# Performance work log

Hardware: AMD Instinct MI355X
Metric: run time of the kernel (lower is better)

The kernel has to match this reference:

```python
import jax, jax.numpy as jnp
import numpy as np

NROW = 200000
R = 32
B = 131072
NDIM = 3
STEP = 0.01  # stepsize from optimize() default step=lambda x: 0.01


def setup_inputs() -> dict:
    key = jax.random.key(0)
    ks = jax.random.split(key, 12)
    inp = {}
    for d in range(NDIM):
        # positive entries (like torch.rand) keep phi > 0
        inp[f"U{d}"] = jax.random.uniform(ks[d], (NROW, R), dtype=jnp.float32, minval=0.05, maxval=1.0)
        inp[f"S{d}"] = jax.random.uniform(ks[3 + d], (NROW, R), dtype=jnp.float32)
        inp[f"T{d}"] = jax.random.uniform(ks[6 + d], (NROW, R), dtype=jnp.float32)
    inp["L"] = jax.random.uniform(ks[9], (R,), dtype=jnp.float32, minval=0.1, maxval=1.0)
    inp["batch_vals"] = jax.random.randint(ks[10], (B,), 0, 2).astype(jnp.float32)  # binary data
    inp["batch_entries"] = jax.random.randint(ks[11], (B, NDIM), 0, NROW)
    return inp


def _em_update(U, S, T, L, batch_vals, batch_entries):
    # U, S, T: (ndim, nrow, R); batch_entries: (B, ndim); batch_vals: (B,)
    idx = batch_entries.T  # (ndim, B)
    g = jax.vmap(lambda u, i: u[i])(U, idx)  # gathered rows: (ndim, B, R)
    # c_vectors[dim] = L * prod of OTHER dims' gathered vectors
    prod_others = jnp.stack([g[1] * g[2], g[0] * g[2], g[0] * g[1]])  # (ndim, B, R)
    c = L * prod_others  # (ndim, B, R)
    p = g[0] * g[1] * g[2]  # (B, R) full elementwise product
    phi = jnp.sum(L * p, axis=-1)  # (B,)
    # d_vectors[dim, b, r] = phi[b] - L[r] * p[b, r]  (same for every dim)
    d_vec = (phi[:, None] - L * p)[None]  # (1, B, R)
    # expectation step (binary): E[wi] = 0.5/phi * tanh(phi/2)
    wi = 0.5 / phi * jnp.tanh(phi / 2.0)  # (B,)
    ki = batch_vals - 0.5  # (B,)
    wi_b = wi[None, :, None]
    s_upd = c * c * wi_b  # (ndim, B, R)
    t_upd = (ki[None, :, None] - d_vec * wi_b) * c  # (ndim, B, R)
    seg = lambda dat, i: jax.ops.segment_sum(dat, i, num_segments=NROW)
    s_acc = jax.vmap(seg)(s_upd, idx)  # (ndim, NROW, R)
    t_acc = jax.vmap(seg)(t_upd, idx)
    cnt = jax.vmap(seg)(jnp.ones(idx.shape, jnp.float32), idx)  # (ndim, NROW)
    touched = (cnt > 0)[..., None]
    # EMA write-back only to rows that appeared in the batch
    S_new = jnp.where(touched, (1.0 - STEP) * S + STEP * s_acc, S)
    T_new = jnp.where(touched, (1.0 - STEP) * T + STEP * t_acc, T)
    return jnp.stack([S_new, T_new])  # (2, ndim, NROW, R)


def reference(U0, U1, U2, S0, S1, S2, T0, T1, T2, L, batch_vals, batch_entries):
    U = jnp.stack([U0, U1, U2])
    S = jnp.stack([S0, S1, S2])
    T = jnp.stack([T0, T1, T2])
    return _em_update(U, S, T, L, batch_vals, batch_entries)
```

## Files before the change

### kernel.cpp

```cpp
#include <hip/hip_runtime.h>

#define NROW 200000
#define RDIM 32
#define BATCH 131072
#define STEP 0.01f


__global__ __launch_bounds__(256) void em_pre(
    const float* __restrict__ U0, const float* __restrict__ U1,
    const float* __restrict__ U2, const float* __restrict__ L,
    const float* __restrict__ bv, const int* __restrict__ be,
    int* __restrict__ head, int* __restrict__ nxt,
    float2* __restrict__ scal, float* __restrict__ LpBuf)
{
    int tid = blockIdx.x * blockDim.x + threadIdx.x;
    int i   = tid >> 3;
    int sub = tid & 7;
    if (i >= BATCH) return;

    int e0 = be[i * 3 + 0];
    int e1 = be[i * 3 + 1];
    int e2 = be[i * 3 + 2];

    float4 g0 = *(const float4*)(U0 + (size_t)e0 * RDIM + sub * 4);
    float4 g1 = *(const float4*)(U1 + (size_t)e1 * RDIM + sub * 4);
    float4 g2 = *(const float4*)(U2 + (size_t)e2 * RDIM + sub * 4);
    float4 Lv = *(const float4*)(L + sub * 4);

    float4 Lp;
    Lp.x = Lv.x * g0.x * g1.x * g2.x;
    Lp.y = Lv.y * g0.y * g1.y * g2.y;
    Lp.z = Lv.z * g0.z * g1.z * g2.z;
    Lp.w = Lv.w * g0.w * g1.w * g2.w;

    float phi = (Lp.x + Lp.y) + (Lp.z + Lp.w);
    phi += __shfl_xor(phi, 1);
    phi += __shfl_xor(phi, 2);
    phi += __shfl_xor(phi, 4);

    float wi = 0.5f / phi * tanhf(0.5f * phi);

    *(float4*)(LpBuf + (size_t)i * RDIM + sub * 4) = Lp;

    if (sub == 0) {
        float A = (bv[i] - 0.5f) - phi * wi;
        scal[i] = make_float2(A, wi);
    }
    if (sub < 3) {
        int row = (sub == 0) ? e0 : (sub == 1) ? e1 : e2;
        int idx = i * 3 + sub;
        nxt[idx] = atomicExch(&head[sub * NROW + row], idx);
    }
}

__global__ __launch_bounds__(256) void em_apply_vec(
    const float* __restrict__ U0, const float* __restrict__ U1,
    const float* __restrict__ U2,
    const float* __restrict__ S0, const float* __restrict__ S1,
    const float* __restrict__ S2,
    const float* __restrict__ T0, const float* __restrict__ T1,
    const float* __restrict__ T2,
    const int* __restrict__ head, const int* __restrict__ nxt,
    const float2* __restrict__ scal, const float* __restrict__ LpBuf,
    float* __restrict__ out)
{
    int tid = blockIdx.x * blockDim.x + threadIdx.x;
    int rid = tid >> 3;
    int sub = tid & 7;
    if (rid >= 3 * NROW) return;

    int d   = rid / NROW;
    int row = rid - d * NROW;

    const float* Ud   = (d == 0) ? U0 : (d == 1) ? U1 : U2;
    const float* Ssrc = (d == 0) ? S0 : (d == 1) ? S1 : S2;
    const float* Tsrc = (d == 0) ? T0 : (d == 1) ? T1 : T2;

    size_t roff = (size_t)row * RDIM + sub * 4;
    float4 s_in = *(const float4*)(Ssrc + roff);
    float4 t_in = *(const float4*)(Tsrc + roff);

    int    t    = head[rid];
    float4 oS   = s_in;
    float4 oT   = t_in;

    if (t != -1) {
        float4 gd = *(const float4*)(Ud + roff);
        float4 rg;
        rg.x = __builtin_amdgcn_rcpf(gd.x);
        rg.y = __builtin_amdgcn_rcpf(gd.y);
        rg.z = __builtin_amdgcn_rcpf(gd.z);
        rg.w = __builtin_amdgcn_rcpf(gd.w);

        float4 sa = make_float4(0.f, 0.f, 0.f, 0.f);
        float4 ta = make_float4(0.f, 0.f, 0.f, 0.f);
        while (t != -1) {
            int e = t / 3;
            float2 aw = scal[e];
            float4 Lp = *(const float4*)(LpBuf + (size_t)e * RDIM + sub * 4);
            float cx = Lp.x * rg.x, cy = Lp.y * rg.y,
                  cz = Lp.z * rg.z, cw = Lp.w * rg.w;
            sa.x += aw.y * cx * cx;  sa.y += aw.y * cy * cy;
            sa.z += aw.y * cz * cz;  sa.w += aw.y * cw * cw;
            ta.x += (aw.x + aw.y * Lp.x) * cx;
            ta.y += (aw.x + aw.y * Lp.y) * cy;
            ta.z += (aw.x + aw.y * Lp.z) * cz;
            ta.w += (aw.x + aw.y * Lp.w) * cw;
            t = nxt[t];
        }
        oS.x = (1.0f - STEP) * s_in.x + STEP * sa.x;
        oS.y = (1.0f - STEP) * s_in.y + STEP * sa.y;
        oS.z = (1.0f - STEP) * s_in.z + STEP * sa.z;
        oS.w = (1.0f - STEP) * s_in.w + STEP * sa.w;
        oT.x = (1.0f - STEP) * t_in.x + STEP * ta.x;
        oT.y = (1.0f - STEP) * t_in.y + STEP * ta.y;
        oT.z = (1.0f - STEP) * t_in.z + STEP * ta.z;
        oT.w = (1.0f - STEP) * t_in.w + STEP * ta.w;
    }

    size_t offS = ((size_t)d * NROW + row) * RDIM + sub * 4;
    *(float4*)(out + offS) = oS;
    *(float4*)(out + (size_t)3 * NROW * RDIM + offS) = oT;
}

__global__ __launch_bounds__(256) void em_build(
    const int* __restrict__ be, int* __restrict__ head, int* __restrict__ nxt)
{
    int tid = blockIdx.x * blockDim.x + threadIdx.x;
    if (tid >= BATCH * 3) return;
    int d   = tid % 3;
    int row = be[tid];
    nxt[tid] = atomicExch(&head[d * NROW + row], tid);
}

__global__ __launch_bounds__(256) void em_gather(
    const float* __restrict__ U0, const float* __restrict__ U1,
    const float* __restrict__ U2,
    const float* __restrict__ S0, const float* __restrict__ S1,
    const float* __restrict__ S2,
    const float* __restrict__ T0, const float* __restrict__ T1,
    const float* __restrict__ T2,
    const float* __restrict__ L,  const float* __restrict__ bv,
    const int* __restrict__ be,
    const int* __restrict__ head, const int* __restrict__ nxt,
    float* __restrict__ out)
{
    int gid   = blockIdx.x * blockDim.x + threadIdx.x;
    int group = gid >> 5;
    int lane  = gid & 31;
    if (group >= 3 * NROW) return;

    int d   = group / NROW;
    int row = group - d * NROW;

    const float* Ud  = (d == 0) ? U0 : (d == 1) ? U1 : U2;
    const float* Uo1 = (d == 0) ? U1 : U0;
    const float* Uo2 = (d == 2) ? U1 : U2;
    int o1 = (d == 0) ? 1 : 0;
    int o2 = (d == 2) ? 1 : 2;
    const float* Ssrc = (d == 0) ? S0 : (d == 1) ? S1 : S2;
    const float* Tsrc = (d == 0) ? T0 : (d == 1) ? T1 : T2;

    size_t row_off = (size_t)row * RDIM + lane;
    float s_in = Ssrc[row_off];
    float t_in = Tsrc[row_off];

    int   t    = head[group];
    float outS = s_in;
    float outT = t_in;

    if (t != -1) {
        float Lr = L[lane];
        float gd = Ud[row_off];
        float sacc = 0.0f, tacc = 0.0f;
        while (t != -1) {
            int e  = t / 3;
            int r1 = be[e * 3 + o1];
            int r2 = be[e * 3 + o2];
            float g1 = Uo1[(size_t)r1 * RDIM + lane];
            float g2 = Uo2[(size_t)r2 * RDIM + lane];
            float ki = bv[e] - 0.5f;

            float c   = Lr * g1 * g2;
            float Lp  = c * gd;
            float phi = Lp;
            #pragma unroll
            for (int m = 1; m < 32; m <<= 1) phi += __shfl_xor(phi, m);

            float wi = 0.5f / phi * tanhf(0.5f * phi);
            sacc += c * c * wi;
            tacc += (ki - (phi - Lp) * wi) * c;

            t = nxt[t];
        }
        outS = (1.0f - STEP) * s_in + STEP * sacc;
        outT = (1.0f - STEP) * t_in + STEP * tacc;
    }

    size_t offS = ((size_t)d * NROW + row) * RDIM + lane;
    out[offS] = outS;
    out[(size_t)3 * NROW * RDIM + offS] = outT;
}

extern "C" void kernel_launch(void* const* d_in, const int* in_sizes, int n_in,
                              void* d_out, int out_size, void* d_ws, size_t ws_size,
                              hipStream_t stream)
{
    const float* U0 = (const float*)d_in[0];
    const float* S0 = (const float*)d_in[1];
    const float* T0 = (const float*)d_in[2];
    const float* U1 = (const float*)d_in[3];
    const float* S1 = (const float*)d_in[4];
    const float* T1 = (const float*)d_in[5];
    const float* U2 = (const float*)d_in[6];
    const float* S2 = (const float*)d_in[7];
    const float* T2 = (const float*)d_in[8];
    const float* L  = (const float*)d_in[9];
    const float* bv = (const float*)d_in[10];
    const int*   be = (const int*)d_in[11];

    float* out = (float*)d_out;

    const size_t head_n = (size_t)3 * NROW;
    const size_t nxt_n  = (size_t)3 * BATCH;
    const size_t ws_fast = (head_n + nxt_n) * sizeof(int)
                         + (size_t)BATCH * sizeof(float2)
                         + (size_t)BATCH * RDIM * sizeof(float);

    int* head_ = (int*)d_ws;
    int* nxt   = head_ + head_n;

    hipMemsetAsync(head_, 0xFF, head_n * sizeof(int), stream);

    if (ws_size >= ws_fast) {
        float2* scal  = (float2*)(nxt + nxt_n);
        float*  LpBuf = (float*)(scal + BATCH);

        int pblocks = (BATCH * 8 + 255) / 256;
        em_pre<<<pblocks, 256, 0, stream>>>(U0, U1, U2, L, bv, be,
                                            head_, nxt, scal, LpBuf);

        long athreads = 3L * NROW * 8;
        int  ablocks  = (int)((athreads + 255) / 256);
        em_apply_vec<<<ablocks, 256, 0, stream>>>(U0, U1, U2, S0, S1, S2,
                                                  T0, T1, T2, head_, nxt,
                                                  scal, LpBuf, out);
    } else {
        int bblocks = (BATCH * 3 + 255) / 256;
        em_build<<<bblocks, 256, 0, stream>>>(be, head_, nxt);

        long gthreads = 3L * NROW * 32;
        int  gblocks  = (int)((gthreads + 255) / 256);
        em_gather<<<gblocks, 256, 0, stream>>>(U0, U1, U2, S0, S1, S2,
                                               T0, T1, T2, L, bv, be,
                                               head_, nxt, out);
    }
}
```

Baseline: 107.8 us.

## Replace per-row linked lists with fixed-capacity buckets plus overflow chain

Builds per-row fixed-capacity buckets (up to 8 batch indices) via atomicAdd counters during the precompute pass, falling back to the existing linked list only for overflow entries. The apply kernel iterates the bucket contiguously instead of chasing nxt pointers, meant to remove dependent-load latency. It adds an extra memset for counters and a larger workspace footprint, and drops the low-workspace gather fallback path.

Measured after the change: 118.9 us. 10.3% more time.

```diff
diff --git a/kernel.cpp b/kernel.cpp
--- a/kernel.cpp
+++ b/kernel.cpp
@@ -4,7 +4,151 @@
 #define RDIM 32
 #define BATCH 131072
 #define STEP 0.01f
-
+#define CAP 8
+
+
+__global__ __launch_bounds__(256) void em_pre_bkt(
+    const float* __restrict__ U0, const float* __restrict__ U1,
+    const float* __restrict__ U2, const float* __restrict__ L,
+    const float* __restrict__ bv, const int* __restrict__ be,
+    int* __restrict__ cnt, int* __restrict__ head, int* __restrict__ nxt,
+    int* __restrict__ bucket, float2* __restrict__ scal, float* __restrict__ LpBuf)
+{
+    int tid = blockIdx.x * blockDim.x + threadIdx.x;
+    int i   = tid >> 3;
+    int sub = tid & 7;
+    if (i >= BATCH) return;
+
+    int e0 = be[i * 3 + 0];
+    int e1 = be[i * 3 + 1];
+    int e2 = be[i * 3 + 2];
+
+    float4 g0 = *(const float4*)(U0 + (size_t)e0 * RDIM + sub * 4);
+    float4 g1 = *(const float4*)(U1 + (size_t)e1 * RDIM + sub * 4);
+    float4 g2 = *(const float4*)(U2 + (size_t)e2 * RDIM + sub * 4);
+    float4 Lv = *(const float4*)(L + sub * 4);
+
+    float4 Lp;
+    Lp.x = Lv.x * g0.x * g1.x * g2.x;
+    Lp.y = Lv.y * g0.y * g1.y * g2.y;
+    Lp.z = Lv.z * g0.z * g1.z * g2.z;
+    Lp.w = Lv.w * g0.w * g1.w * g2.w;
+
+    float phi = (Lp.x + Lp.y) + (Lp.z + Lp.w);
+    phi += __shfl_xor(phi, 1);
+    phi += __shfl_xor(phi, 2);
+    phi += __shfl_xor(phi, 4);
+
+    float wi = 0.5f / phi * tanhf(0.5f * phi);
+
+    *(float4*)(LpBuf + (size_t)i * RDIM + sub * 4) = Lp;
+
+    if (sub == 0) {
+        float A = (bv[i] - 0.5f) - phi * wi;
+        scal[i] = make_float2(A, wi);
+    }
+    if (sub < 3) {
+        int row = (sub == 0) ? e0 : (sub == 1) ? e1 : e2;
+        int rid = sub * NROW + row;
+        int slot = atomicAdd(&cnt[rid], 1);
+        if (slot < CAP) {
+            bucket[(size_t)rid * CAP + slot] = i;
+        } else {
+            int idx = i * 3 + sub;
+            nxt[idx] = atomicExch(&head[rid], idx);
+        }
+    }
+}
+
+__global__ __launch_bounds__(256) void em_apply_bkt(
+    const float* __restrict__ U0, const float* __restrict__ U1,
+    const float* __restrict__ U2,
+    const float* __restrict__ S0, const float* __restrict__ S1,
+    const float* __restrict__ S2,
+    const float* __restrict__ T0, const float* __restrict__ T1,
+    const float* __restrict__ T2,
+    const int* __restrict__ cnt, const int* __restrict__ head,
+    const int* __restrict__ nxt, const int* __restrict__ bucket,
+    const float2* __restrict__ scal, const float* __restrict__ LpBuf,
+    float* __restrict__ out)
+{
+    int tid = blockIdx.x * blockDim.x + threadIdx.x;
+    int rid = tid >> 3;
+    int sub = tid & 7;
+    if (rid >= 3 * NROW) return;
+
+    int d   = rid / NROW;
+    int row = rid - d * NROW;
+
+    const float* Ud   = (d == 0) ? U0 : (d == 1) ? U1 : U2;
+    const float* Ssrc = (d == 0) ? S0 : (d == 1) ? S1 : S2;
+    const float* Tsrc = (d == 0) ? T0 : (d == 1) ? T1 : T2;
+
+    size_t roff = (size_t)row * RDIM + sub * 4;
+    float4 s_in = *(const float4*)(Ssrc + roff);
+    float4 t_in = *(const float4*)(Tsrc + roff);
+
+    int    n  = cnt[rid];
+    float4 oS = s_in;
+    float4 oT = t_in;
+
+    if (n > 0) {
+        float4 gd = *(const float4*)(Ud + roff);
+        float4 rg;
+        rg.x = __builtin_amdgcn_rcpf(gd.x);
+        rg.y = __builtin_amdgcn_rcpf(gd.y);
+        rg.z = __builtin_amdgcn_rcpf(gd.z);
+        rg.w = __builtin_amdgcn_rcpf(gd.w);
+
+        float4 sa = make_float4(0.f, 0.f, 0.f, 0.f);
+        float4 ta = make_float4(0.f, 0.f, 0.f, 0.f);
+
+        const int* bk = bucket + (size_t)rid * CAP;
+        int nb = (n < CAP) ? n : CAP;
+        for (int j = 0; j < nb; ++j) {
+            int e = bk[j];
+            float2 aw = scal[e];
+            float4 Lp = *(const float4*)(LpBuf + (size_t)e * RDIM + sub * 4);
+            float cx = Lp.x * rg.x, cy = Lp.y * rg.y,
+                  cz = Lp.z * rg.z, cw = Lp.w * rg.w;
+            sa.x += aw.y * cx * cx;  sa.y += aw.y * cy * cy;
+            sa.z += aw.y * cz * cz;  sa.w += aw.y * cw * cw;
+            ta.x += (aw.x + aw.y * Lp.x) * cx;
+            ta.y += (aw.x + aw.y * Lp.y) * cy;
+            ta.z += (aw.x + aw.y * Lp.z) * cz;
+            ta.w += (aw.x + aw.y * Lp.w) * cw;
+        }
+        if (n > CAP) {
+            int t = head[rid];
+            while (t != -1) {
+                int e = t / 3;
+                float2 aw = scal[e];
+                float4 Lp = *(const float4*)(LpBuf + (size_t)e * RDIM + sub * 4);
+                float cx = Lp.x * rg.x, cy = Lp.y * rg.y,
+                      cz = Lp.z * rg.z, cw = Lp.w * rg.w;
+                sa.x += aw.y * cx * cx;  sa.y += aw.y * cy * cy;
+                sa.z += aw.y * cz * cz;  sa.w += aw.y * cw * cw;
+                ta.x += (aw.x + aw.y * Lp.x) * cx;
+                ta.y += (aw.x + aw.y * Lp.y) * cy;
+                ta.z += (aw.x + aw.y * Lp.z) * cz;
+                ta.w += (aw.x + aw.y * Lp.w) * cw;
+                t = nxt[t];
+            }
+        }
+        oS.x = (1.0f - STEP) * s_in.x + STEP * sa.x;
+        oS.y = (1.0f - STEP) * s_in.y + STEP * sa.y;
+        oS.z = (1.0f - STEP) * s_in.z + STEP * sa.z;
+        oS.w = (1.0f - STEP) * s_in.w + STEP * sa.w;
+        oT.x = (1.0f - STEP) * t_in.x + STEP * ta.x;
+        oT.y = (1.0f - STEP) * t_in.y + STEP * ta.y;
+        oT.z = (1.0f - STEP) * t_in.z + STEP * ta.z;
+        oT.w = (1.0f - STEP) * t_in.w + STEP * ta.w;
+    }
+
+    size_t offS = ((size_t)d * NROW + row) * RDIM + sub * 4;
+    *(float4*)(out + offS) = oS;
+    *(float4*)(out + (size_t)3 * NROW * RDIM + offS) = oT;
+}
 
 __global__ __launch_bounds__(256) void em_pre(
     const float* __restrict__ U0, const float* __restrict__ U1,
@@ -80,9 +224,9 @@
     float4 s_in = *(const float4*)(Ssrc + roff);
     float4 t_in = *(const float4*)(Tsrc + roff);
 
-    int    t    = head[rid];
-    float4 oS   = s_in;
-    float4 oT   = t_in;
+    int    t  = head[rid];
+    float4 oS = s_in;
+    float4 oT = t_in;
 
     if (t != -1) {
         float4 gd = *(const float4*)(Ud + roff);
@@ -123,85 +267,6 @@
     *(float4*)(out + (size_t)3 * NROW * RDIM + offS) = oT;
 }
 
-__global__ __launch_bounds__(256) void em_build(
-    const int* __restrict__ be, int* __restrict__ head, int* __restrict__ nxt)
-{
-    int tid = blockIdx.x * blockDim.x + threadIdx.x;
-    if (tid >= BATCH * 3) return;
-    int d   = tid % 3;
-    int row = be[tid];
-    nxt[tid] = atomicExch(&head[d * NROW + row], tid);
-}
-
-__global__ __launch_bounds__(256) void em_gather(
-    const float* __restrict__ U0, const float* __restrict__ U1,
-    const float* __restrict__ U2,
-    const float* __restrict__ S0, const float* __restrict__ S1,
-    const float* __restrict__ S2,
-    const float* __restrict__ T0, const float* __restrict__ T1,
-    const float* __restrict__ T2,
-    const float* __restrict__ L,  const float* __restrict__ bv,
-    const int* __restrict__ be,
-    const int* __restrict__ head, const int* __restrict__ nxt,
-    float* __restrict__ out)
-{
-    int gid   = blockIdx.x * blockDim.x + threadIdx.x;
-    int group = gid >> 5;
-    int lane  = gid & 31;
-    if (group >= 3 * NROW) return;
-
-    int d   = group / NROW;
-    int row = group - d * NROW;
-
-    const float* Ud  = (d == 0) ? U0 : (d == 1) ? U1 : U2;
-    const float* Uo1 = (d == 0) ? U1 : U0;
-    const float* Uo2 = (d == 2) ? U1 : U2;
-    int o1 = (d == 0) ? 1 : 0;
-    int o2 = (d == 2) ? 1 : 2;
-    const float* Ssrc = (d == 0) ? S0 : (d == 1) ? S1 : S2;
-    const float* Tsrc = (d == 0) ? T0 : (d == 1) ? T1 : T2;
-
-    size_t row_off = (size_t)row * RDIM + lane;
-    float s_in = Ssrc[row_off];
-    float t_in = Tsrc[row_off];
-
-    int   t    = head[group];
-    float outS = s_in;
-    float outT = t_in;
-
-    if (t != -1) {
-        float Lr = L[lane];
-        float gd = Ud[row_off];
-        float sacc = 0.0f, tacc = 0.0f;
-        while (t != -1) {
-            int e  = t / 3;
-            int r1 = be[e * 3 + o1];
-            int r2 = be[e * 3 + o2];
-            float g1 = Uo1[(size_t)r1 * RDIM + lane];
-            float g2 = Uo2[(size_t)r2 * RDIM + lane];
-            float ki = bv[e] - 0.5f;
-
-            float c   = Lr * g1 * g2;
-            float Lp  = c * gd;
-            float phi = Lp;
-            #pragma unroll
-            for (int m = 1; m < 32; m <<= 1) phi += __shfl_xor(phi, m);
-
-            float wi = 0.5f / phi * tanhf(0.5f * phi);
-            sacc += c * c * wi;
-            tacc += (ki - (phi - Lp) * wi) * c;
-
-            t = nxt[t];
-        }
-        outS = (1.0f - STEP) * s_in + STEP * sacc;
-        outT = (1.0f - STEP) * t_in + STEP * tacc;
-    }
-
-    size_t offS = ((size_t)d * NROW + row) * RDIM + lane;
-    out[offS] = outS;
-    out[(size_t)3 * NROW * RDIM + offS] = outT;
-}
-
 extern "C" void kernel_launch(void* const* d_in, const int* in_sizes, int n_in,
                               void* d_out, int out_size, void* d_ws, size_t ws_size,
                               hipStream_t stream)
@@ -221,20 +286,46 @@
 
     float* out = (float*)d_out;
 
-    const size_t head_n = (size_t)3 * NROW;
+    const size_t rows3  = (size_t)3 * NROW;
     const size_t nxt_n  = (size_t)3 * BATCH;
-    const size_t ws_fast = (head_n + nxt_n) * sizeof(int)
-                         + (size_t)BATCH * sizeof(float2)
-                         + (size_t)BATCH * RDIM * sizeof(float);
-
-    int* head_ = (int*)d_ws;
-    int* nxt   = head_ + head_n;
-
-    hipMemsetAsync(head_, 0xFF, head_n * sizeof(int), stream);
+    const size_t bkt_n  = rows3 * CAP;
+
+    const size_t ints_fast = rows3  + rows3  + nxt_n + bkt_n;
+    const size_t ws_fast   = ints_fast * sizeof(int)
+                           + (size_t)BATCH * sizeof(float2)
+                           + (size_t)BATCH * RDIM * sizeof(float);
+    const size_t ws_mid    = (rows3 + nxt_n) * sizeof(int)
+                           + (size_t)BATCH * sizeof(float2)
+                           + (size_t)BATCH * RDIM * sizeof(float);
 
     if (ws_size >= ws_fast) {
+        int*    cnt    = (int*)d_ws;
+        int*    head_  = cnt + rows3;
+        int*    nxt    = head_ + rows3;
+        int*    bucket = nxt + nxt_n;
+        float2* scal   = (float2*)(bucket + bkt_n);
+        float*  LpBuf  = (float*)(scal + BATCH);
+
+        hipMemsetAsync(cnt, 0, rows3 * sizeof(int), stream);
+        hipMemsetAsync(head_, 0xFF, rows3 * sizeof(int), stream);
+
+        int pblocks = (BATCH * 8 + 255) / 256;
+        em_pre_bkt<<<pblocks, 256, 0, stream>>>(U0, U1, U2, L, bv, be,
+                                                cnt, head_, nxt, bucket,
+                                                scal, LpBuf);
+
+        long athreads = 3L * NROW * 8;
+        int  ablocks  = (int)((athreads + 255) / 256);
+        em_apply_bkt<<<ablocks, 256, 0, stream>>>(U0, U1, U2, S0, S1, S2,
+                                                  T0, T1, T2, cnt, head_, nxt,
+                                                  bucket, scal, LpBuf, out);
+    } else if (ws_size >= ws_mid) {
+        int*    head_ = (int*)d_ws;
+        int*    nxt   = head_ + rows3;
         float2* scal  = (float2*)(nxt + nxt_n);
         float*  LpBuf = (float*)(scal + BATCH);
+
+        hipMemsetAsync(head_, 0xFF, rows3 * sizeof(int), stream);
 
         int pblocks = (BATCH * 8 + 255) / 256;
         em_pre<<<pblocks, 256, 0, stream>>>(U0, U1, U2, L, bv, be,
@@ -245,14 +336,5 @@
         em_apply_vec<<<ablocks, 256, 0, stream>>>(U0, U1, U2, S0, S1, S2,
                                                   T0, T1, T2, head_, nxt,
                                                   scal, LpBuf, out);
-    } else {
-        int bblocks = (BATCH * 3 + 255) / 256;
-        em_build<<<bblocks, 256, 0, stream>>>(be, head_, nxt);
-
-        long gthreads = 3L * NROW * 32;
-        int  gblocks  = (int)((gthreads + 255) / 256);
-        em_gather<<<gblocks, 256, 0, stream>>>(U0, U1, U2, S0, S1, S2,
-                                               T0, T1, T2, L, bv, be,
-                                               head_, nxt, out);
-    }
-}
+    }
+}
```
